# Kernel optimization log

Hardware: AMD Instinct MI355X
Metric: run time of the kernel (lower is better)

The kernel has to match this reference:

```python
import jax, jax.numpy as jnp
import numpy as np

NUM_HEADS = 16

def setup_inputs() -> dict:
    key = jax.random.key(0)
    ks = jax.random.split(key, 7)
    B, S, D = 2, 2048, 1024
    X = jax.random.normal(ks[0], (B, S, D), dtype=jnp.float32)
    s = 1.0 / np.sqrt(D)
    Wq = jax.random.normal(ks[1], (D, D), dtype=jnp.float32) * s
    Wk = jax.random.normal(ks[2], (D, D), dtype=jnp.float32) * s
    Wv = jax.random.normal(ks[3], (D, D), dtype=jnp.float32) * s
    Wo = jax.random.normal(ks[4], (D, D), dtype=jnp.float32) * s
    bo = jnp.zeros((D,), dtype=jnp.float32)
    return {"X": X, "Wq": Wq, "Wk": Wk, "Wv": Wv, "Wo": Wo, "bo": bo}

def reference(X, Wq, Wk, Wv, Wo, bo):
    B, S, D = X.shape
    H = NUM_HEADS
    hd = D // H
    # project and split heads -> [B, H, S, hd]
    def split(t):
        return t.reshape(B, S, H, hd).transpose(0, 2, 1, 3)
    q = split(X @ Wq)
    k = split(X @ Wk)
    v = split(X @ Wv)
    scores = jnp.einsum('bhqd,bhkd->bhqk', q, k) / jnp.sqrt(jnp.float32(hd))
    causal = jnp.tril(jnp.ones((S, S), dtype=bool))
    scores = jnp.where(causal, scores, -jnp.inf)
    weights = jax.nn.softmax(scores, axis=-1)  # dropout p=0 -> identity
    ctx = jnp.einsum('bhqk,bhkd->bhqd', weights, v)
    ctx = ctx.transpose(0, 2, 1, 3).reshape(B, S, D)
    return ctx @ Wo + bo
```

## Files before the change

kernel.cpp:

```cpp
#include <hip/hip_runtime.h>


typedef __attribute__((ext_vector_type(8))) short short8;
typedef __attribute__((ext_vector_type(4))) float floatx4;

__device__ inline unsigned short f2bf(float f) {
  unsigned u = __float_as_uint(f);
  unsigned r = (u + 0x7fffu + ((u >> 16) & 1u)) >> 16;
  return (unsigned short)r;
}

__device__ __forceinline__ float fast_exp2(float x) {
#if __has_builtin(__builtin_amdgcn_exp2f)
  return __builtin_amdgcn_exp2f(x);
#else
  float r;
  asm volatile("v_exp_f32_e32 %0, %1" : "=v"(r) : "v"(x));
  return r;
#endif
}

__device__ __forceinline__ void gll16(const unsigned short* g, unsigned short* l) {
  __builtin_amdgcn_global_load_lds(
      (const __attribute__((address_space(1))) unsigned int*)(g),
      (__attribute__((address_space(3))) unsigned int*)(l),
      16, 0, 0);
}

constexpr int B_ = 2, S_ = 2048, D_ = 1024, H_ = 16, HD_ = 64;

__global__ __launch_bounds__(256) void prep_inputs(
    const float* __restrict__ x, unsigned short* __restrict__ xb,
    const float* __restrict__ w0, const float* __restrict__ w1,
    const float* __restrict__ w2, const float* __restrict__ w3,
    unsigned short* __restrict__ wt_base)
{
  if (blockIdx.z == 4) {
    const int tid = threadIdx.y * 32 + threadIdx.x;
    const size_t base =
        ((size_t)(blockIdx.y * 32 + blockIdx.x) * 256 + tid) * 16;
#pragma unroll
    for (int half = 0; half < 2; ++half) {
      const size_t i = base + half * 8;
      float4 a = *(const float4*)(x + i);
      float4 b = *(const float4*)(x + i + 4);
      short8 o;
      o[0] = (short)f2bf(a.x); o[1] = (short)f2bf(a.y);
      o[2] = (short)f2bf(a.z); o[3] = (short)f2bf(a.w);
      o[4] = (short)f2bf(b.x); o[5] = (short)f2bf(b.y);
      o[6] = (short)f2bf(b.z); o[7] = (short)f2bf(b.w);
      *(short8*)(xb + i) = o;
    }
    return;
  }
  const float* src;
  switch (blockIdx.z) {
    case 0: src = w0; break;
    case 1: src = w1; break;
    case 2: src = w2; break;
    default: src = w3; break;
  }
  unsigned short* dst = wt_base + (size_t)blockIdx.z * 1024 * 1024;
  __shared__ unsigned short t[32][33];
  const int bx = blockIdx.x * 32;
  const int by = blockIdx.y * 32;
  const int x_ = threadIdx.x;
  for (int yy = threadIdx.y; yy < 32; yy += 8)
    t[yy][x_] = f2bf(src[(size_t)(by + yy) * 1024 + bx + x_]);
  __syncthreads();
  for (int yy = threadIdx.y; yy < 32; yy += 8)
    dst[(size_t)(bx + yy) * 1024 + by + x_] = t[x_][yy];
}

__global__ __launch_bounds__(256) void transpose_v(
    const unsigned short* __restrict__ Vb, unsigned short* __restrict__ Vt)
{
  __shared__ unsigned short t[32][33];
  const int bh = blockIdx.z;
  const int b = bh >> 4, h = bh & 15;
  const int s0 = blockIdx.x * 32, d0 = blockIdx.y * 32;
  const int x = threadIdx.x;
  for (int yy = threadIdx.y; yy < 32; yy += 8)
    t[yy][x] = Vb[(size_t)(b * 2048 + s0 + yy) * 1024 + h * 64 + d0 + x];
  __syncthreads();
  for (int yy = threadIdx.y; yy < 32; yy += 8)
    Vt[((size_t)bh * 64 + d0 + yy) * 2048 + s0 + x] = t[x][yy];
}

__global__ __launch_bounds__(256) void gemm256_qkv(
    const unsigned short* __restrict__ A,
    const unsigned short* __restrict__ Bt,
    unsigned short* __restrict__ Qo,
    unsigned short* __restrict__ Ko,
    unsigned short* __restrict__ Vo)
{
  __shared__ unsigned short sA[2][128 * 32];
  __shared__ unsigned short sB[2][128 * 32];
  const int K = 1024;

  const int L = blockIdx.y * 24 + blockIdx.x;
  const int rid = (L & 7) * 96 + (L >> 3);
  const int brow = rid / 24, bcol = rid % 24;
  const int m0 = brow * 128;
  const int bn0 = bcol * 128;

  const int tid = threadIdx.x, wave = tid >> 6, lane = tid & 63;
  const int g = lane >> 4, ml = lane & 15;
  const int wm = wave & 1, wn = wave >> 1;

  const unsigned short* ag0 = A + (size_t)(m0 + (tid >> 2)) * K + (tid & 3) * 8;
  const unsigned short* ag1 = ag0 + (size_t)64 * K;
  const unsigned short* bg0 = Bt + (size_t)(bn0 + (tid >> 2)) * K + (tid & 3) * 8;
  const unsigned short* bg1 = bg0 + (size_t)64 * K;
  const int woff = wave * 512;

  floatx4 acc[4][4];
#pragma unroll
  for (int mt = 0; mt < 4; ++mt)
#pragma unroll
    for (int nt = 0; nt < 4; ++nt) acc[mt][nt] = (floatx4){0.f, 0.f, 0.f, 0.f};

  for (int k0 = 0; k0 < K; k0 += 64) {
    __syncthreads();
#pragma unroll
    for (int t = 0; t < 2; ++t) {
      gll16(ag0 + k0 + t * 32, sA[t] + woff);
      gll16(ag1 + k0 + t * 32, sA[t] + 2048 + woff);
      gll16(bg0 + k0 + t * 32, sB[t] + woff);
      gll16(bg1 + k0 + t * 32, sB[t] + 2048 + woff);
    }
    __syncthreads();
#pragma unroll
    for (int t = 0; t < 2; ++t) {
      short8 af[4], bf[4];
#pragma unroll
      for (int mt = 0; mt < 4; ++mt)
        af[mt] = *(const short8*)(sA[t] + (wm * 64 + mt * 16 + ml) * 32 + g * 8);
#pragma unroll
      for (int nt = 0; nt < 4; ++nt)
        bf[nt] = *(const short8*)(sB[t] + (wn * 64 + nt * 16 + ml) * 32 + g * 8);
#pragma unroll
      for (int mt = 0; mt < 4; ++mt)
#pragma unroll
        for (int nt = 0; nt < 4; ++nt)
          acc[mt][nt] = __builtin_amdgcn_mfma_f32_16x16x32_bf16(
              af[mt], bf[nt], acc[mt][nt], 0, 0, 0);
    }
  }

  const int proj = bcol >> 3;
  unsigned short* out = (proj == 0) ? Qo : (proj == 1) ? Ko : Vo;
  const int col0 = (bcol & 7) * 128;
#pragma unroll
  for (int mt = 0; mt < 4; ++mt) {
#pragma unroll
    for (int nt = 0; nt < 4; ++nt) {
      const int col = col0 + wn * 64 + nt * 16 + ml;
#pragma unroll
      for (int r = 0; r < 4; ++r) {
        const int row = m0 + wm * 64 + mt * 16 + g * 4 + r;
        out[(size_t)row * 1024 + col] = f2bf(acc[mt][nt][r]);
      }
    }
  }
}

__global__ __launch_bounds__(256) void gemm_wo64(
    const unsigned short* __restrict__ A,
    const unsigned short* __restrict__ Bt,
    const float* __restrict__ bias,
    float* __restrict__ C)
{
  __shared__ unsigned short sA[4][64 * 32];
  __shared__ unsigned short sB[4][128 * 32];
  const int K = 1024;

  const int L = blockIdx.y * 8 + blockIdx.x;
  const int rid = (L & 7) * 64 + (L >> 3);
  const int m0 = (rid >> 3) * 64;
  const int bn0 = (rid & 7) * 128;

  const int tid = threadIdx.x, wave = tid >> 6, lane = tid & 63;
  const int g = lane >> 4, ml = lane & 15;
  const int wm = wave & 1, wn = wave >> 1;

  const unsigned short* ag =
      A + (size_t)(m0 + wave * 16 + (lane >> 2)) * K + (lane & 3) * 8;
  const unsigned short* bg0 = Bt + (size_t)(bn0 + (tid >> 2)) * K + (tid & 3) * 8;
  const unsigned short* bg1 = bg0 + (size_t)64 * K;
  const int woff = wave * 512;

  floatx4 acc[2][4];
#pragma unroll
  for (int mt = 0; mt < 2; ++mt)
#pragma unroll
    for (int nt = 0; nt < 4; ++nt) acc[mt][nt] = (floatx4){0.f, 0.f, 0.f, 0.f};

  for (int k0 = 0; k0 < K; k0 += 128) {
    __syncthreads();
#pragma unroll
    for (int t = 0; t < 4; ++t) {
      gll16(ag + k0 + t * 32, sA[t] + woff);
      gll16(bg0 + k0 + t * 32, sB[t] + woff);
      gll16(bg1 + k0 + t * 32, sB[t] + 2048 + woff);
    }
    __syncthreads();
#pragma unroll
    for (int t = 0; t < 4; ++t) {
      short8 af[2], bf[4];
#pragma unroll
      for (int mt = 0; mt < 2; ++mt)
        af[mt] = *(const short8*)(sA[t] + (wm * 32 + mt * 16 + ml) * 32 + g * 8);
#pragma unroll
      for (int nt = 0; nt < 4; ++nt)
        bf[nt] = *(const short8*)(sB[t] + (wn * 64 + nt * 16 + ml) * 32 + g * 8);
#pragma unroll
      for (int mt = 0; mt < 2; ++mt)
#pragma unroll
        for (int nt = 0; nt < 4; ++nt)
          acc[mt][nt] = __builtin_amdgcn_mfma_f32_16x16x32_bf16(
              af[mt], bf[nt], acc[mt][nt], 0, 0, 0);
    }
  }

#pragma unroll
  for (int mt = 0; mt < 2; ++mt) {
#pragma unroll
    for (int nt = 0; nt < 4; ++nt) {
      const int col = bn0 + wn * 64 + nt * 16 + ml;
      const float badd = bias[col];
#pragma unroll
      for (int r = 0; r < 4; ++r) {
        const int row = m0 + wm * 32 + mt * 16 + g * 4 + r;
        C[(size_t)row * 1024 + col] = acc[mt][nt][r] + badd;
      }
    }
  }
}

constexpr int KTPB = 2;

struct AttnLds {
  unsigned short k0[2][KTPB][64 * 32];
  unsigned short k1[2][KTPB][64 * 32];
  unsigned short v0[2][KTPB][64 * 32];
  unsigned short v1[2][KTPB][64 * 32];
};
union __align__(16) AttnLdsU {
  AttnLds t;
  float comb[4 * 64 * 36];
};

__device__ __forceinline__ void softmax_pack(
    const floatx4* s, const bool diag, const int qg, const int kb,
    float& l, short8* ap)
{
  const float C1 = 0.18033688f;
  const float C2 = -34.6246810f;

  unsigned wb[4][4];
  float lp0 = 0.f, lp1 = 0.f, lp2 = 0.f, lp3 = 0.f;
#pragma unroll
  for (int nb = 0; nb < 4; ++nb) {
#pragma unroll
    for (int r = 0; r < 4; ++r) {
      float wv = fast_exp2(fmaf(s[nb][r], C1, C2));
      if (diag && (kb + nb * 16 + r > qg)) wv = 0.f;
      wb[nb][r] = __float_as_uint(wv);
      if (nb == 0) lp0 += wv;
      else if (nb == 1) lp1 += wv;
      else if (nb == 2) lp2 += wv;
      else lp3 += wv;
    }
  }
  l += (lp0 + lp1) + (lp2 + lp3);

  unsigned pk[4][2];
#pragma unroll
  for (int nb = 0; nb < 4; ++nb) {
    pk[nb][0] = __builtin_amdgcn_perm(wb[nb][1], wb[nb][0], 0x07060302u);
    pk[nb][1] = __builtin_amdgcn_perm(wb[nb][3], wb[nb][2], 0x07060302u);
  }

  unsigned Fr[2][4];
#pragma unroll
  for (int rr = 0; rr < 2; ++rr) {
    unsigned a0 = pk[0][rr], a1 = pk[1][rr];
    unsigned a2 = pk[2][rr], a3 = pk[3][rr];
    asm("v_permlane32_swap_b32 %0, %1" : "+v"(a0), "+v"(a1));
    asm("v_permlane32_swap_b32 %0, %1" : "+v"(a2), "+v"(a3));
    asm("v_permlane16_swap_b32 %0, %1" : "+v"(a0), "+v"(a1));
    asm("v_permlane16_swap_b32 %0, %1" : "+v"(a2), "+v"(a3));
    Fr[0][rr] = a0; Fr[0][2 + rr] = a1;
    Fr[1][rr] = a2; Fr[1][2 + rr] = a3;
  }
#pragma unroll
  for (int f = 0; f < 2; ++f) {
    union { unsigned u[4]; short8 s8; } uap;
    uap.u[0] = Fr[f][0]; uap.u[1] = Fr[f][1];
    uap.u[2] = Fr[f][2]; uap.u[3] = Fr[f][3];
    ap[f] = uap.s8;
  }
}

template <bool DUAL>
__device__ __forceinline__ void attn_tile2(
    const short8* aqB, const short8* aqA,
    const unsigned short* sK0, const unsigned short* sK1,
    const unsigned short* sV0, const unsigned short* sV1,
    floatx4* accB, float& lB, floatx4* accA, float& lA,
    const bool diagB, const bool diagA,
    const int qgB, const int qgA, const int kb,
    const int g, const int ml)
{
  floatx4 sB[4], sA[4];
  __builtin_amdgcn_s_setprio(1);
#pragma unroll
  for (int nb = 0; nb < 4; ++nb) {
    short8 bk0 = *(const short8*)(sK0 + (nb * 16 + ml) * 32 + g * 8);
    short8 bk1 = *(const short8*)(sK1 + (nb * 16 + ml) * 32 + g * 8);
    sB[nb] = (floatx4){0.f, 0.f, 0.f, 0.f};
    sB[nb] = __builtin_amdgcn_mfma_f32_16x16x32_bf16(bk0, aqB[0], sB[nb], 0, 0, 0);
    sB[nb] = __builtin_amdgcn_mfma_f32_16x16x32_bf16(bk1, aqB[1], sB[nb], 0, 0, 0);
    if (DUAL) {
      sA[nb] = (floatx4){0.f, 0.f, 0.f, 0.f};
      sA[nb] = __builtin_amdgcn_mfma_f32_16x16x32_bf16(bk0, aqA[0], sA[nb], 0, 0, 0);
      sA[nb] = __builtin_amdgcn_mfma_f32_16x16x32_bf16(bk1, aqA[1], sA[nb], 0, 0, 0);
    }
  }
  __builtin_amdgcn_s_setprio(0);

  short8 apB[2], apA[2];
  softmax_pack(sB, diagB, qgB, kb, lB, apB);
  if (DUAL) softmax_pack(sA, diagA, qgA, kb, lA, apA);

  __builtin_amdgcn_s_setprio(1);
#pragma unroll
  for (int f = 0; f < 2; ++f) {
    const unsigned short* sv = f ? sV1 : sV0;
#pragma unroll
    for (int jd = 0; jd < 4; ++jd) {
      short8 bv = *(const short8*)(sv + (jd * 16 + ml) * 32 + g * 8);
      accB[jd] = __builtin_amdgcn_mfma_f32_16x16x32_bf16(apB[f], bv, accB[jd], 0, 0, 0);
      if (DUAL)
        accA[jd] = __builtin_amdgcn_mfma_f32_16x16x32_bf16(apA[f], bv, accA[jd], 0, 0, 0);
    }
  }
  __builtin_amdgcn_s_setprio(0);
}

__global__ __launch_bounds__(512) void attn_v16(
    const unsigned short* __restrict__ Q,
    const unsigned short* __restrict__ Kg,
    const unsigned short* __restrict__ Vt,
    unsigned short* __restrict__ CTX)
{
  __shared__ AttnLdsU lds;

  const int L = blockIdx.x;
  const int rid = (L & 7) * 64 + (L >> 3);
  const int p = rid & 15;
  const int bh = rid >> 4;

  const int b = bh >> 4, h = bh & 15;
  const int qbA = p, qbB = 31 - p;
  const int qA0 = qbA * 64, qB0 = qbB * 64;
  const int tid = threadIdx.x, w = tid >> 6, lane = tid & 63;
  const int slice = w & 3, par = w >> 2;
  const int g = lane >> 4, ml = lane & 15;

  const size_t headoff = (size_t)b * S_ * D_ + (size_t)h * HD_;
  const size_t vtoff   = (size_t)bh * HD_ * S_;

  short8 aqA[2], aqB[2];
  {
    const unsigned short* qp =
        Q + headoff + (size_t)(qA0 + slice * 16 + ml) * D_ + g * 8;
    aqA[0] = *(const short8*)qp;
    aqA[1] = *(const short8*)(qp + 32);
  }
  {
    const unsigned short* qp =
        Q + headoff + (size_t)(qB0 + slice * 16 + ml) * D_ + g * 8;
    aqB[0] = *(const short8*)qp;
    aqB[1] = *(const short8*)(qp + 32);
  }

  floatx4 accA[4], accB[4];
#pragma unroll
  for (int jd = 0; jd < 4; ++jd) {
    accA[jd] = (floatx4){0.f, 0.f, 0.f, 0.f};
    accB[jd] = (floatx4){0.f, 0.f, 0.f, 0.f};
  }
  float lA = 0.f, lB = 0.f;
  const int qgA = qA0 + slice * 16 + ml;
  const int qgB = qB0 + slice * 16 + ml;

  const int sw = slice;
  const unsigned short* kgb =
      Kg + headoff + (size_t)(sw * 16 + (lane >> 2)) * D_ + (lane & 3) * 8;
  const unsigned short* vgb =
      Vt + vtoff + (size_t)(sw * 16 + (lane >> 2)) * S_ + (lane & 3) * 8;
  const int woff = sw * 512;

  const int ntiles = qbB + 1;

  {
    const int cnt = (ntiles < KTPB) ? ntiles : KTPB;
#pragma unroll
    for (int t = 0; t < KTPB; ++t) {
      if (t >= cnt) break;
      if (w < 4) {
        const size_t ko = (size_t)t * 64 * D_;
        gll16(kgb + ko,      lds.t.k0[0][t] + woff);
        gll16(kgb + ko + 32, lds.t.k1[0][t] + woff);
      } else {
        gll16(vgb + t * 64,      lds.t.v0[0][t] + woff);
        gll16(vgb + t * 64 + 32, lds.t.v1[0][t] + woff);
      }
    }
  }
  __syncthreads();

  for (int kt0 = 0; kt0 < ntiles; kt0 += KTPB) {
    const int bufi = (kt0 >> 1) & 1;
    const int nxt = kt0 + KTPB;
    if (nxt < ntiles) {
      const int cn = (ntiles - nxt < KTPB) ? (ntiles - nxt) : KTPB;
#pragma unroll
      for (int t = 0; t < KTPB; ++t) {
        if (t >= cn) break;
        const int kt = nxt + t;
        if (w < 4) {
          const size_t ko = (size_t)kt * 64 * D_;
          gll16(kgb + ko,      lds.t.k0[bufi ^ 1][t] + woff);
          gll16(kgb + ko + 32, lds.t.k1[bufi ^ 1][t] + woff);
        } else {
          gll16(vgb + kt * 64,      lds.t.v0[bufi ^ 1][t] + woff);
          gll16(vgb + kt * 64 + 32, lds.t.v1[bufi ^ 1][t] + woff);
        }
      }
    }

    const int cnt = (ntiles - kt0 < KTPB) ? (ntiles - kt0) : KTPB;
    if (par < cnt) {
      const int kt = kt0 + par;
      const int kb = kt * 64 + g * 4;
      if (kt <= qbA)
        attn_tile2<true>(aqB, aqA,
                         lds.t.k0[bufi][par], lds.t.k1[bufi][par],
                         lds.t.v0[bufi][par], lds.t.v1[bufi][par],
                         accB, lB, accA, lA,
                         kt == qbB, kt == qbA, qgB, qgA, kb, g, ml);
      else
        attn_tile2<false>(aqB, aqA,
                          lds.t.k0[bufi][par], lds.t.k1[bufi][par],
                          lds.t.v0[bufi][par], lds.t.v1[bufi][par],
                          accB, lB, accA, lA,
                          kt == qbB, false, qgB, qgA, kb, g, ml);
    }
    __syncthreads();
  }

  {
    float* slot = lds.comb + (size_t)(slice * 64 + lane) * 36;
    if (par == 1) {
#pragma unroll
      for (int jd = 0; jd < 4; ++jd) {
        *(floatx4*)(slot + jd * 4) = accA[jd];
        *(floatx4*)(slot + 16 + jd * 4) = accB[jd];
      }
      slot[32] = lA;
      slot[33] = lB;
    }
    __syncthreads();
    if (par == 1) return;
#pragma unroll
    for (int jd = 0; jd < 4; ++jd) {
      accA[jd] += *(const floatx4*)(slot + jd * 4);
      accB[jd] += *(const floatx4*)(slot + 16 + jd * 4);
    }
    lA += slot[32];
    lB += slot[33];
  }

  lA += __shfl_xor(lA, 16); lA += __shfl_xor(lA, 32);
  lB += __shfl_xor(lB, 16); lB += __shfl_xor(lB, 32);
  const float liA = 1.0f / lA;
  const float liB = 1.0f / lB;
  float lrA[4], lrB[4];
#pragma unroll
  for (int r = 0; r < 4; ++r) {
    lrA[r] = __shfl(liA, g * 4 + r);
    lrB[r] = __shfl(liB, g * 4 + r);
  }

#pragma unroll
  for (int r = 0; r < 4; ++r) {
    const int rowA = qA0 + slice * 16 + g * 4 + r;
    const int rowB = qB0 + slice * 16 + g * 4 + r;
#pragma unroll
    for (int jd = 0; jd < 4; ++jd) {
      CTX[headoff + (size_t)rowA * D_ + jd * 16 + ml] = f2bf(accA[jd][r] * lrA[r]);
      CTX[headoff + (size_t)rowB * D_ + jd * 16 + ml] = f2bf(accB[jd][r] * lrB[r]);
    }
  }
}

extern "C" void kernel_launch(void* const* d_in, const int* in_sizes, int n_in,
                              void* d_out, int out_size, void* d_ws, size_t ws_size,
                              hipStream_t stream)
{
  const float* X  = (const float*)d_in[0];
  const float* Wq = (const float*)d_in[1];
  const float* Wk = (const float*)d_in[2];
  const float* Wv = (const float*)d_in[3];
  const float* Wo = (const float*)d_in[4];
  const float* bo = (const float*)d_in[5];

  char* ws = (char*)d_ws;
  const size_t MB = 1024 * 1024;

  unsigned short* Qb  = (unsigned short*)(ws);
  unsigned short* Kb  = (unsigned short*)(ws + 8 * MB);
  unsigned short* Xb  = (unsigned short*)(ws + 16 * MB);
  unsigned short* WT  = (unsigned short*)(ws + 24 * MB);
  unsigned short* WoT = WT + (size_t)3 * 1024 * 1024;
  unsigned short* Vb  = (unsigned short*)d_out;
  unsigned short* Vt  = Xb;

  prep_inputs<<<dim3(32, 32, 5), dim3(32, 8), 0, stream>>>(
      X, Xb, Wq, Wk, Wv, Wo, WT);
  gemm256_qkv<<<dim3(24, 32), 256, 0, stream>>>(Xb, WT, Qb, Kb, Vb);
  transpose_v<<<dim3(64, 2, 32), dim3(32, 8), 0, stream>>>(Vb, Vt);
  attn_v16<<<dim3(512), 512, 0, stream>>>(Qb, Kb, Vt, Qb);
  gemm_wo64<<<dim3(8, 64), 256, 0, stream>>>(Qb, WoT, bo, (float*)d_out);
}
```

Measured before the change: 183.6 us.

## Load V tiles directly from global into registers instead of staging through LDS

The attention kernel no longer stages V tiles in shared memory. Each wave now reads its V fragments straight from global (transposed V) into registers at the start of each tile, and all 8 waves share the K async loads. This halves LDS use and removes the LDS round trip for V. In exchange, every wave that handles the same tile re-reads V from global/L2, and those loads are not prefetched a tile ahead, so their latency may be exposed before the PV MFMAs.

New measurement: 217.9 us. +18.7%, slower.

```diff
diff --git a/kernel.cpp b/kernel.cpp
--- a/kernel.cpp
+++ b/kernel.cpp
@@ -243,8 +243,6 @@
 struct AttnLds {
   unsigned short k0[2][KTPB][64 * 32];
   unsigned short k1[2][KTPB][64 * 32];
-  unsigned short v0[2][KTPB][64 * 32];
-  unsigned short v1[2][KTPB][64 * 32];
 };
 union __align__(16) AttnLdsU {
   AttnLds t;
@@ -307,12 +305,19 @@
 __device__ __forceinline__ void attn_tile2(
     const short8* aqB, const short8* aqA,
     const unsigned short* sK0, const unsigned short* sK1,
-    const unsigned short* sV0, const unsigned short* sV1,
+    const unsigned short* vtile,
     floatx4* accB, float& lB, floatx4* accA, float& lA,
     const bool diagB, const bool diagA,
     const int qgB, const int qgA, const int kb,
     const int g, const int ml)
 {
+  short8 vb[2][4];
+#pragma unroll
+  for (int f = 0; f < 2; ++f)
+#pragma unroll
+    for (int jd = 0; jd < 4; ++jd)
+      vb[f][jd] = *(const short8*)(vtile + (size_t)jd * 16 * 2048 + f * 32);
+
   floatx4 sB[4], sA[4];
   __builtin_amdgcn_s_setprio(1);
 #pragma unroll
@@ -337,19 +342,17 @@
   __builtin_amdgcn_s_setprio(1);
 #pragma unroll
   for (int f = 0; f < 2; ++f) {
-    const unsigned short* sv = f ? sV1 : sV0;
 #pragma unroll
     for (int jd = 0; jd < 4; ++jd) {
-      short8 bv = *(const short8*)(sv + (jd * 16 + ml) * 32 + g * 8);
-      accB[jd] = __builtin_amdgcn_mfma_f32_16x16x32_bf16(apB[f], bv, accB[jd], 0, 0, 0);
+      accB[jd] = __builtin_amdgcn_mfma_f32_16x16x32_bf16(apB[f], vb[f][jd], accB[jd], 0, 0, 0);
       if (DUAL)
-        accA[jd] = __builtin_amdgcn_mfma_f32_16x16x32_bf16(apA[f], bv, accA[jd], 0, 0, 0);
+        accA[jd] = __builtin_amdgcn_mfma_f32_16x16x32_bf16(apA[f], vb[f][jd], accA[jd], 0, 0, 0);
     }
   }
   __builtin_amdgcn_s_setprio(0);
 }
 
-__global__ __launch_bounds__(512) void attn_v16(
+__global__ __launch_bounds__(512) void attn_v17(
     const unsigned short* __restrict__ Q,
     const unsigned short* __restrict__ Kg,
     const unsigned short* __restrict__ Vt,
@@ -396,29 +399,20 @@
   const int qgA = qA0 + slice * 16 + ml;
   const int qgB = qB0 + slice * 16 + ml;
 
-  const int sw = slice;
+  const int st = w & 1;
+  const int srb = w >> 1;
   const unsigned short* kgb =
-      Kg + headoff + (size_t)(sw * 16 + (lane >> 2)) * D_ + (lane & 3) * 8;
-  const unsigned short* vgb =
-      Vt + vtoff + (size_t)(sw * 16 + (lane >> 2)) * S_ + (lane & 3) * 8;
-  const int woff = sw * 512;
+      Kg + headoff + (size_t)(srb * 16 + (lane >> 2)) * D_ + (lane & 3) * 8;
+  const int woff = srb * 512;
+
+  const unsigned short* vbase = Vt + vtoff + (size_t)ml * S_ + g * 8;
 
   const int ntiles = qbB + 1;
 
-  {
-    const int cnt = (ntiles < KTPB) ? ntiles : KTPB;
-#pragma unroll
-    for (int t = 0; t < KTPB; ++t) {
-      if (t >= cnt) break;
-      if (w < 4) {
-        const size_t ko = (size_t)t * 64 * D_;
-        gll16(kgb + ko,      lds.t.k0[0][t] + woff);
-        gll16(kgb + ko + 32, lds.t.k1[0][t] + woff);
-      } else {
-        gll16(vgb + t * 64,      lds.t.v0[0][t] + woff);
-        gll16(vgb + t * 64 + 32, lds.t.v1[0][t] + woff);
-      }
-    }
+  if (st < ((ntiles < KTPB) ? ntiles : KTPB)) {
+    const size_t ko = (size_t)st * 64 * D_;
+    gll16(kgb + ko,      lds.t.k0[0][st] + woff);
+    gll16(kgb + ko + 32, lds.t.k1[0][st] + woff);
   }
   __syncthreads();
 
@@ -427,18 +421,10 @@
     const int nxt = kt0 + KTPB;
     if (nxt < ntiles) {
       const int cn = (ntiles - nxt < KTPB) ? (ntiles - nxt) : KTPB;
-#pragma unroll
-      for (int t = 0; t < KTPB; ++t) {
-        if (t >= cn) break;
-        const int kt = nxt + t;
-        if (w < 4) {
-          const size_t ko = (size_t)kt * 64 * D_;
-          gll16(kgb + ko,      lds.t.k0[bufi ^ 1][t] + woff);
-          gll16(kgb + ko + 32, lds.t.k1[bufi ^ 1][t] + woff);
-        } else {
-          gll16(vgb + kt * 64,      lds.t.v0[bufi ^ 1][t] + woff);
-          gll16(vgb + kt * 64 + 32, lds.t.v1[bufi ^ 1][t] + woff);
-        }
+      if (st < cn) {
+        const size_t ko = (size_t)(nxt + st) * 64 * D_;
+        gll16(kgb + ko,      lds.t.k0[bufi ^ 1][st] + woff);
+        gll16(kgb + ko + 32, lds.t.k1[bufi ^ 1][st] + woff);
       }
     }
 
@@ -446,16 +432,15 @@
     if (par < cnt) {
       const int kt = kt0 + par;
       const int kb = kt * 64 + g * 4;
+      const unsigned short* vtile = vbase + kt * 64;
       if (kt <= qbA)
         attn_tile2<true>(aqB, aqA,
-                         lds.t.k0[bufi][par], lds.t.k1[bufi][par],
-                         lds.t.v0[bufi][par], lds.t.v1[bufi][par],
+                         lds.t.k0[bufi][par], lds.t.k1[bufi][par], vtile,
                          accB, lB, accA, lA,
                          kt == qbB, kt == qbA, qgB, qgA, kb, g, ml);
       else
         attn_tile2<false>(aqB, aqA,
-                          lds.t.k0[bufi][par], lds.t.k1[bufi][par],
-                          lds.t.v0[bufi][par], lds.t.v1[bufi][par],
+                          lds.t.k0[bufi][par], lds.t.k1[bufi][par], vtile,
                           accB, lB, accA, lA,
                           kt == qbB, false, qgB, qgA, kb, g, ml);
     }
@@ -533,6 +518,6 @@
       X, Xb, Wq, Wk, Wv, Wo, WT);
   gemm256_qkv<<<dim3(24, 32), 256, 0, stream>>>(Xb, WT, Qb, Kb, Vb);
   transpose_v<<<dim3(64, 2, 32), dim3(32, 8), 0, stream>>>(Vb, Vt);
-  attn_v16<<<dim3(512), 512, 0, stream>>>(Qb, Kb, Vt, Qb);
+  attn_v17<<<dim3(512), 512, 0, stream>>>(Qb, Kb, Vt, Qb);
   gemm_wo64<<<dim3(8, 64), 256, 0, stream>>>(Qb, WoT, bo, (float*)d_out);
 }
```
